# Performance work log

Measured on AMD Instinct MI355X. Metric: run time of the kernel, lower is better.

## Reference

```python
import jax, jax.numpy as jnp
from jax import lax
import numpy as np

HIDDEN = 4096
HEADS = 32
HEAD_DIM = HIDDEN // HEADS  # 128
STATE = 16
K = 3  # short_filter_length
B, L = 2, 4096


def setup_inputs() -> dict:
    key = jax.random.key(0)
    k0, k1, k2, k3, k4, k5 = jax.random.split(key, 6)
    u = jax.random.normal(k0, (B, L, 3 * HIDDEN), dtype=jnp.float32)
    short_filter_weight = jax.random.normal(k1, (3 * HIDDEN, 1, K), dtype=jnp.float32)
    short_filter_bias = jax.random.normal(k2, (3 * HIDDEN,), dtype=jnp.float32)
    D = 0.1 * jax.random.normal(k3, (HIDDEN,), dtype=jnp.float32)
    # poles[...,0] = 0.01*randn, poles[...,1] = 0.001*randn (as in __init__)
    poles = jnp.stack(
        [0.01 * jax.random.normal(k4, (1, STATE, 1), dtype=jnp.float32),
         0.001 * jax.random.normal(jax.random.fold_in(k4, 1), (1, STATE, 1), dtype=jnp.float32)],
        axis=-1)
    residues = jax.random.normal(k5, (1, STATE, 1, 2), dtype=jnp.float32)
    return {"u": u, "short_filter_weight": short_filter_weight,
            "short_filter_bias": short_filter_bias, "D": D,
            "poles": poles, "residues": residues}


def reference(u, short_filter_weight, short_filter_bias, D, poles, residues):
    Bsz, Lq, threeD = u.shape
    hidden = threeD // 3
    # ---- parallel FIR: causal depthwise conv over [B, 3D, L] ----
    x = jnp.transpose(u, (0, 2, 1))  # [B, 3D, L]
    z_pre = lax.conv_general_dilated(
        x, short_filter_weight, window_strides=(1,), padding=[(K - 1, 0)],
        feature_group_count=threeD, dimension_numbers=("NCH", "OIH", "NCH"))
    z_pre = z_pre + short_filter_bias[None, :, None]  # [B, 3D, L]
    # ---- column split (column_split_hyena=True) ----
    z = z_pre.reshape(Bsz, HEADS, 3 * HEAD_DIM, Lq)
    x2 = z[:, :, :HEAD_DIM].reshape(Bsz, hidden, Lq)
    x1 = z[:, :, HEAD_DIM:2 * HEAD_DIM].reshape(Bsz, hidden, Lq)
    v = z[:, :, 2 * HEAD_DIM:].reshape(Bsz, hidden, Lq)
    x1v = x1 * v  # [B, D, L]
    # ---- pole/residue filter: h[t] = Re(sum_s r_s * p_s^t) ----
    t = jnp.arange(Lq, dtype=jnp.float32)[None, None, :]  # [1, 1, L]
    pc = (poles[..., 0] + 1j * poles[..., 1]).astype(jnp.complex64)      # [1, S, 1]
    rc = (residues[..., 0] + 1j * residues[..., 1]).astype(jnp.complex64)
    log_poles = jnp.log(pc)
    h = (rc * jnp.exp(log_poles * t)).real.sum(axis=1)[None]  # [1, 1, L]
    # ---- FFT long convolution (prefill_style='fft') ----
    fft_size = 2 * Lq
    Hf = jnp.fft.rfft(h.astype(jnp.float32), n=fft_size) / fft_size      # [1, 1, L+1]
    Xs = jnp.fft.fft(x1v.astype(jnp.float32), n=fft_size)                # [B, D, 2L]
    X = Xs[..., : Hf.shape[-1]]
    y = jnp.fft.irfft(X * Hf, n=fft_size, norm="forward")[..., :Lq]      # [B, D, L]
    # ---- skip + output gate ----
    y = (y + x1v * D[None, :, None]) * x2
    return jnp.transpose(y, (0, 2, 1))  # [B, L, D]
```

## Files before the change

kernel.cpp:

```cpp
#include <hip/hip_runtime.h>
#include <hip/hip_bf16.h>


#define HID    4096
#define THREED 12288
#define LSEQ   4096
#define TAPS   16
#define TT     128
#define NST    16
#define SUB    8

__global__ __launch_bounds__(256, 2) void hyena_fused(
    const float* __restrict__ u,
    const float* __restrict__ sfw,
    const float* __restrict__ sfb,
    const float* __restrict__ Dp,
    const float* __restrict__ poles,
    const float* __restrict__ residues,
    float* __restrict__ out)
{
    const int tid = threadIdx.x;
    const int ib  = blockIdx.x & 15;
    const int tc  = (blockIdx.x >> 4) & 31;
    const int b   = blockIdx.x >> 9;
    const int i   = (ib << 8) + tid;
    const int head = i >> 7;
    const int j    = i & 127;
    const int c2 = head * 384 + j;
    const int c1 = c2 + 128;
    const int cv = c2 + 256;

    const float w1a = sfw[c1*3+0], w1b = sfw[c1*3+1], w1c = sfw[c1*3+2], b1 = sfb[c1];
    const float wva = sfw[cv*3+0], wvb = sfw[cv*3+1], wvc = sfw[cv*3+2], bv = sfb[cv];
    const float w2a = sfw[c2*3+0], w2b = sfw[c2*3+1], w2c = sfw[c2*3+2], b2 = sfb[c2];
    const float Dc  = Dp[i];

    float h[TAPS];
#pragma unroll
    for (int t = 0; t < TAPS; ++t) h[t] = 0.f;
#pragma unroll 1
    for (int s = 0; s < NST; ++s) {
        const float pr = poles[2*s],    pim = poles[2*s+1];
        float cr = residues[2*s], ci = residues[2*s+1];
#pragma unroll
        for (int t = 0; t < TAPS; ++t) {
            h[t] += cr;
            const float nr = cr*pr - ci*pim;
            const float ni = cr*pim + ci*pr;
            cr = nr; ci = ni;
        }
    }
#pragma unroll
    for (int t = 0; t < TAPS; ++t)
        h[t] = __uint_as_float(__builtin_amdgcn_readfirstlane(__float_as_uint(h[t])));

    const int t0 = tc * TT;
    const int rowBase = b * LSEQ;

    auto ldu = [&](int t, int c) -> float {
        return (t >= 0) ? u[(size_t)(rowBase + t) * THREED + c] : 0.f;
    };

    float u1m2 = ldu(t0-17, c1), u1m1 = ldu(t0-16, c1);
    float uvm2 = ldu(t0-17, cv), uvm1 = ldu(t0-16, cv);

    float xw[16];
    xw[0] = 0.f;
#pragma unroll
    for (int k = 1; k < 16; ++k) {
        const int t = t0 - 16 + k;
        const float a1 = ldu(t, c1);
        const float av = ldu(t, cv);
        const float z1 = fmaf(w1c, a1, fmaf(w1b, u1m1, fmaf(w1a, u1m2, b1)));
        const float zv = fmaf(wvc, av, fmaf(wvb, uvm1, fmaf(wva, uvm2, bv)));
        xw[k] = (t >= 0) ? z1 * zv : 0.f;
        u1m2 = u1m1; u1m1 = a1;
        uvm2 = uvm1; uvm1 = av;
    }
    float u2m2 = ldu(t0-2, c2), u2m1 = ldu(t0-1, c2);

    const float* __restrict__ urow = u   + (size_t)(rowBase + t0) * THREED;
    float*       __restrict__ orow = out + (size_t)(rowBase + t0) * HID + i;

    for (int g = 0; g < TT/16; ++g) {
#pragma unroll
        for (int half = 0; half < 2; ++half) {
            float a1[SUB], av[SUB], a2[SUB];
#pragma unroll
            for (int p = 0; p < SUB; ++p) {
                const float* row = urow + (size_t)(g*16 + half*SUB + p) * THREED;
                a1[p] = row[c1];
                av[p] = row[cv];
                a2[p] = row[c2];
            }
#pragma unroll
            for (int p = 0; p < SUB; ++p) {
                const int q = half*SUB + p;
                const float z1 = fmaf(w1c, a1[p], fmaf(w1b, u1m1, fmaf(w1a, u1m2, b1)));
                const float zv = fmaf(wvc, av[p], fmaf(wvb, uvm1, fmaf(wva, uvm2, bv)));
                const float z2 = fmaf(w2c, a2[p], fmaf(w2b, u2m1, fmaf(w2a, u2m2, b2)));
                const float x1v = z1 * zv;
                xw[q] = x1v;
                float acc = x1v * Dc;
#pragma unroll
                for (int tau = 0; tau < TAPS; ++tau)
                    acc = fmaf(h[tau], xw[(q - tau) & 15], acc);
                orow[(size_t)(g*16 + q) * HID] = acc * z2;
                u1m2 = u1m1; u1m1 = a1[p];
                uvm2 = uvm1; uvm1 = av[p];
                u2m2 = u2m1; u2m1 = a2[p];
            }
        }
    }
}

extern "C" void kernel_launch(void* const* d_in, const int* in_sizes, int n_in,
                              void* d_out, int out_size, void* d_ws, size_t ws_size,
                              hipStream_t stream) {
    const float* u        = (const float*)d_in[0];
    const float* sfw      = (const float*)d_in[1];
    const float* sfb      = (const float*)d_in[2];
    const float* Dp       = (const float*)d_in[3];
    const float* poles    = (const float*)d_in[4];
    const float* residues = (const float*)d_in[5];
    float* out = (float*)d_out;

    hyena_fused<<<dim3(1024), dim3(256), 0, stream>>>(
        u, sfw, sfb, Dp, poles, residues, out);
}
```

Before: 576.3 us.

## Stage input rows through double-buffered LDS with async global_load_lds

Per-thread scalar strided loads of the three conv input channels are replaced by cooperative 16-byte global_load_lds transfers. Each block copies its contiguous 768-column segment for 8 timesteps into a double-buffered LDS tile. The next chunk is prefetched while the current one is computed, with s_waitcnt/barrier synchronisation between chunks, and output stores are made nontemporal. This aims to raise effective load bandwidth and overlap memory latency with the FIR/filter compute, at the cost of extra LDS use and block-wide barriers.

```diff
diff --git a/kernel.cpp b/kernel.cpp
--- a/kernel.cpp
+++ b/kernel.cpp
@@ -1,5 +1,4 @@
 #include <hip/hip_runtime.h>
-#include <hip/hip_bf16.h>
 
 
 #define HID    4096
@@ -8,7 +7,12 @@
 #define TAPS   16
 #define TT     128
 #define NST    16
-#define SUB    8
+#define CHUNK  8
+#define NCHK   (TT/CHUNK)
+#define SEG    768
+
+typedef __attribute__((address_space(1))) const void glb_void;
+typedef __attribute__((address_space(3))) void       lds_void;
 
 __global__ __launch_bounds__(256, 2) void hyena_fused(
     const float* __restrict__ u,
@@ -19,16 +23,24 @@
     const float* __restrict__ residues,
     float* __restrict__ out)
 {
-    const int tid = threadIdx.x;
-    const int ib  = blockIdx.x & 15;
-    const int tc  = (blockIdx.x >> 4) & 31;
-    const int b   = blockIdx.x >> 9;
-    const int i   = (ib << 8) + tid;
-    const int head = i >> 7;
-    const int j    = i & 127;
-    const int c2 = head * 384 + j;
-    const int c1 = c2 + 128;
-    const int cv = c2 + 256;
+    __shared__ float lds[2][CHUNK][SEG];
+
+    const int tid  = threadIdx.x;
+    const int lane = tid & 63;
+    const int wv   = tid >> 6;
+    const int ib   = blockIdx.x & 15;
+    const int tc   = (blockIdx.x >> 4) & 31;
+    const int b    = blockIdx.x >> 9;
+    const int i    = (ib << 8) + tid;
+    const int hl   = tid >> 7;
+    const int j    = tid & 127;
+    const int o2 = hl * 384 + j;
+    const int o1 = o2 + 128;
+    const int ov = o2 + 256;
+    const int cbase = ib * 768;
+    const int c2 = cbase + o2;
+    const int c1 = cbase + o1;
+    const int cv = cbase + ov;
 
     const float w1a = sfw[c1*3+0], w1b = sfw[c1*3+1], w1c = sfw[c1*3+2], b1 = sfb[c1];
     const float wva = sfw[cv*3+0], wvb = sfw[cv*3+1], wvc = sfw[cv*3+2], bv = sfb[cv];
@@ -79,39 +91,61 @@
     }
     float u2m2 = ldu(t0-2, c2), u2m1 = ldu(t0-1, c2);
 
-    const float* __restrict__ urow = u   + (size_t)(rowBase + t0) * THREED;
+    const float* __restrict__ useg = u   + (size_t)(rowBase + t0) * THREED + cbase;
     float*       __restrict__ orow = out + (size_t)(rowBase + t0) * HID + i;
 
-    for (int g = 0; g < TT/16; ++g) {
+    auto stage = [&](int bi, int cidx) {
+        const float* gs = useg + (size_t)(cidx * CHUNK + 2 * wv) * THREED + lane * 4;
+        float* ls = &lds[bi][2 * wv][0];
 #pragma unroll
-        for (int half = 0; half < 2; ++half) {
-            float a1[SUB], av[SUB], a2[SUB];
+        for (int rr = 0; rr < 2; ++rr) {
 #pragma unroll
-            for (int p = 0; p < SUB; ++p) {
-                const float* row = urow + (size_t)(g*16 + half*SUB + p) * THREED;
-                a1[p] = row[c1];
-                av[p] = row[cv];
-                a2[p] = row[c2];
-            }
-#pragma unroll
-            for (int p = 0; p < SUB; ++p) {
-                const int q = half*SUB + p;
-                const float z1 = fmaf(w1c, a1[p], fmaf(w1b, u1m1, fmaf(w1a, u1m2, b1)));
-                const float zv = fmaf(wvc, av[p], fmaf(wvb, uvm1, fmaf(wva, uvm2, bv)));
-                const float z2 = fmaf(w2c, a2[p], fmaf(w2b, u2m1, fmaf(w2a, u2m2, b2)));
-                const float x1v = z1 * zv;
-                xw[q] = x1v;
-                float acc = x1v * Dc;
-#pragma unroll
-                for (int tau = 0; tau < TAPS; ++tau)
-                    acc = fmaf(h[tau], xw[(q - tau) & 15], acc);
-                orow[(size_t)(g*16 + q) * HID] = acc * z2;
-                u1m2 = u1m1; u1m1 = a1[p];
-                uvm2 = uvm1; uvm1 = av[p];
-                u2m2 = u2m1; u2m1 = a2[p];
+            for (int part = 0; part < 3; ++part) {
+                __builtin_amdgcn_global_load_lds(
+                    (glb_void*)(gs + (size_t)rr * THREED + part * 256),
+                    (lds_void*)(ls + rr * SEG + part * 256),
+                    16, 0, 0);
             }
         }
+    };
+
+    stage(0, 0);
+    asm volatile("s_waitcnt vmcnt(0)" ::: "memory");
+    __builtin_amdgcn_s_barrier();
+
+#define DO_CHUNK(C, BI, QB)                                                    \
+    {                                                                          \
+        if ((C) + 1 < NCHK) stage(((C) + 1) & 1, (C) + 1);                     \
+        _Pragma("unroll")                                                      \
+        for (int p = 0; p < CHUNK; ++p) {                                      \
+            const int q = (QB) + p;                                            \
+            const float* Lr = &lds[BI][p][0];                                  \
+            const float a1 = Lr[o1], av = Lr[ov], a2 = Lr[o2];                 \
+            const float z1 = fmaf(w1c, a1, fmaf(w1b, u1m1, fmaf(w1a, u1m2, b1))); \
+            const float zv = fmaf(wvc, av, fmaf(wvb, uvm1, fmaf(wva, uvm2, bv))); \
+            const float z2 = fmaf(w2c, a2, fmaf(w2b, u2m1, fmaf(w2a, u2m2, b2))); \
+            const float x1v = z1 * zv;                                         \
+            xw[q & 15] = x1v;                                                  \
+            float acc = x1v * Dc;                                              \
+            _Pragma("unroll")                                                  \
+            for (int tau = 0; tau < TAPS; ++tau)                               \
+                acc = fmaf(h[tau], xw[(q - tau) & 15], acc);                   \
+            __builtin_nontemporal_store(acc * z2,                              \
+                &orow[(size_t)((C) * CHUNK + p) * HID]);                       \
+            u1m2 = u1m1; u1m1 = a1;                                            \
+            uvm2 = uvm1; uvm1 = av;                                            \
+            u2m2 = u2m1; u2m1 = a2;                                            \
+        }                                                                      \
+        asm volatile("s_waitcnt vmcnt(8)" ::: "memory");                       \
+        __builtin_amdgcn_s_barrier();                                          \
     }
+
+    for (int cp = 0; cp < NCHK / 2; ++cp) {
+        const int ce = 2 * cp;
+        DO_CHUNK(ce,     0, 0)
+        DO_CHUNK(ce + 1, 1, 8)
+    }
+#undef DO_CHUNK
 }
 
 extern "C" void kernel_launch(void* const* d_in, const int* in_sizes, int n_in,
```

After: 574.1 us. About the same (-0.4%).
